# Kernel tuning notes

Hardware: AMD Instinct MI355X
Metric: run time of the kernel (lower is better)

The kernel has to match this reference:

```python
import jax, jax.numpy as jnp
import numpy as np

B, H, L, C, KD, NS = 4, 1024, 8192, 1, 64, 8  # batch, d_model, seq_len, channels, kernel_dim, num_scales
DECAY_MIN, DECAY_MAX = 1.0, 4.0


def _interp_linear(x, scale):
    """F.interpolate(mode='linear', align_corners=False) for integer scale on last axis."""
    if scale == 1:
        return x
    Lin = x.shape[-1]
    Lout = Lin * scale
    pos = (jnp.arange(Lout, dtype=x.dtype) + 0.5) / scale - 0.5
    lo = jnp.floor(pos)
    w = pos - lo  # fractional weight toward hi
    lo_i = jnp.clip(lo.astype(jnp.int32), 0, Lin - 1)
    hi_i = jnp.clip(lo.astype(jnp.int32) + 1, 0, Lin - 1)
    return x[..., lo_i] * (1.0 - w) + x[..., hi_i] * w


def setup_inputs() -> dict:
    key = jax.random.key(0)
    k1, k2, k3, k4 = jax.random.split(key, 4)
    return {
        "u": jax.random.normal(k1, (B, H, L), jnp.float32),
        "kernels": jax.random.normal(k2, (NS, C, H, KD), jnp.float32),
        "D": jax.random.normal(k3, (C, H), jnp.float32),
        "W_out": jax.random.normal(k4, (H, C * H), jnp.float32) / np.sqrt(C * H).astype(np.float32),
        "b_out": jnp.zeros((H,), jnp.float32),
    }


def reference(u, kernels, D, W_out, b_out):
    # --- multi-scale kernel synthesis ('cat' mode, init_scale=0) ---
    mult = jnp.linspace(DECAY_MIN, DECAY_MAX, H).astype(u.dtype).reshape(1, H, 1)
    parts = [
        _interp_linear(kernels[i], 2 ** max(0, i - 1)) * mult ** (NS - 1 - i)
        for i in range(NS)
    ]
    k = jnp.concatenate(parts, axis=-1)  # (C, H, 8192) == (C, H, L) for these dims
    # kernel_norm is computed from the untruncated kernel and detached (buffer)
    knorm = jax.lax.stop_gradient(jnp.linalg.norm(k, axis=-1, keepdims=True))  # (C, H, 1)
    k = k[..., :L] / knorm

    # --- FFT long convolution (causal, via 2L-padded circular conv) ---
    n = 2 * L
    k_f = jnp.fft.rfft(k, n=n)                 # (C, H, L+1) complex
    u_f = jnp.fft.rfft(u, n=n)                 # (B, H, L+1) complex
    y = jnp.fft.irfft(u_f[:, None, :, :] * k_f[None, :, :, :], n=n)[..., :L]  # (B, C, H, L)
    y = y + jnp.einsum('bhl,ch->bchl', u, D)   # skip connection
    y = y.reshape(u.shape[0], C * H, L)        # (B, C*H, L)

    # --- activation + output linear (1x1 conv) ---
    y = jax.nn.gelu(y, approximate=False)      # torch nn.GELU is exact erf form
    y = jnp.einsum('oh,bhl->bol', W_out, y) + b_out[None, :, None]
    return y
```

## Files before the change

### kernel.cpp

```cpp
#include <hip/hip_runtime.h>
#include <hip/hip_bf16.h>

#define LFULL 8192
#define HDIM 1024
#define KPAD 8320

typedef __attribute__((ext_vector_type(8))) short bf16x8;
typedef __attribute__((ext_vector_type(4))) float f32x4;
typedef __attribute__((ext_vector_type(16))) float f32x16;

union U16 {
  uint4 u;
  bf16x8 s;
  ushort e[8];
};

__device__ __forceinline__ ushort f2bf(float x) {
  union { float f; uint u; } a;
  a.f = x;
  uint r = a.u + 0x7fffu + ((a.u >> 16) & 1u);
  return (ushort)(r >> 16);
}
__device__ __forceinline__ float bf2f(ushort x) {
  union { uint u; float f; } a;
  a.u = ((uint)x) << 16;
  return a.f;
}

__device__ __forceinline__ void gload16(const void* src, void* lds) {
  __builtin_amdgcn_global_load_lds(
      (const __attribute__((address_space(1))) unsigned int*)src,
      (__attribute__((address_space(3))) unsigned int*)lds, 16, 0, 0);
}

__device__ __forceinline__ uint ALIGNB(uint hi, uint lo, uint sh) {
#if __has_builtin(__builtin_amdgcn_alignbyte)
  return __builtin_amdgcn_alignbyte(hi, lo, sh);
#else
  return (uint)((((unsigned long long)hi << 32) | (unsigned long long)lo) >> (8u * sh));
#endif
}

__global__ __launch_bounds__(256) void k_synth_kernel(
    const float* __restrict__ kern, ushort* __restrict__ kout) {
  const int h = blockIdx.x;
  const int tid = threadIdx.x;
  __shared__ float Kw[8][64];
  __shared__ __align__(16) float kv[LFULL];
  __shared__ float red[8];
  for (int idx = tid; idx < 8 * 64; idx += 256) {
    int i = idx >> 6, j = idx & 63;
    Kw[i][j] = kern[(i * HDIM + h) * 64 + j];
  }
  __syncthreads();
  const float mult = (float)(1.0 + 3.0 * (double)h / 1023.0);
  float pw[8];
  pw[7] = 1.0f;
#pragma unroll
  for (int i = 6; i >= 0; --i) pw[i] = pw[i + 1] * mult;
  float ss = 0.0f;
  for (int m = tid; m < LFULL; m += 256) {
    const int i = (m < 64) ? 0 : (32 - __clz(m >> 6));
    const int slog = (i == 0) ? 0 : (i - 1);
    const float inv_s = 1.0f / (float)(1 << slog);
    const int off = (i == 0) ? 0 : (64 << (i - 1));
    const int t = m - off;
    const float pos = ((float)t + 0.5f) * inv_s - 0.5f;
    const float lof = floorf(pos);
    const float wgt = pos - lof;
    int lo = (int)lof;
    int hi = lo + 1;
    lo = min(63, max(0, lo));
    hi = min(63, max(0, hi));
    const float val = (Kw[i][lo] * (1.0f - wgt) + Kw[i][hi] * wgt) * pw[i];
    kv[m] = val;
    ss += val * val;
  }
#pragma unroll
  for (int o = 32; o > 0; o >>= 1) ss += __shfl_xor(ss, o, 64);
  if ((tid & 63) == 0) red[tid >> 6] = ss;
  __syncthreads();
  if (tid == 0) red[0] = sqrtf(red[0] + red[1] + red[2] + red[3]);
  __syncthreads();
  const float inv_norm = 1.0f / red[0];
  ushort* krow = kout + (size_t)h * KPAD;
  for (int m = tid; m < LFULL; m += 256) krow[8191 - m] = f2bf(kv[m] * inv_norm);
  if (tid < 128) krow[8192 + tid] = 0;
}

__global__ __launch_bounds__(256, 2) void conv_mfma_kernel(
    const float* __restrict__ u, const ushort* __restrict__ kbrev,
    const float* __restrict__ Dp, ushort* __restrict__ g) {
  __shared__ __align__(16) ushort Us[4 * LFULL];
  __shared__ __align__(16) ushort Ring[4][640];
  const int tid = threadIdx.x;
  const int h = blockIdx.x;
  const int w = tid >> 6;
  const int lane = tid & 63;
  const int c32 = lane & 31;
  const int qh = lane >> 5;
  uint4* Us4 = (uint4*)Us;

  for (int cc = tid; cc < 4096; cc += 256) {
    const int row = cc >> 10, cI = cc & 1023;
    const float* up = u + (((size_t)(row * HDIM + h)) << 13) + (cI << 3);
    const float4 v0 = *(const float4*)up;
    const float4 v1 = *(const float4*)(up + 4);
    U16 pk;
    pk.e[0] = f2bf(v0.x); pk.e[1] = f2bf(v0.y);
    pk.e[2] = f2bf(v0.z); pk.e[3] = f2bf(v0.w);
    pk.e[4] = f2bf(v1.x); pk.e[5] = f2bf(v1.y);
    pk.e[6] = f2bf(v1.z); pk.e[7] = f2bf(v1.w);
    const int phys = (cI & ~7) | ((cI & 7) ^ ((cI >> 3) & 7));
    Us4[(row << 10) + phys] = pk.u;
  }

  const ushort* kr = kbrev + (size_t)h * KPAD;
  ushort* ring = (ushort*)Ring[w];
  {
    const uint k64 = *(const uint*)(kr + 64 * 128 + 2 * lane);
    const uint k63 = *(const uint*)(kr + 63 * 128 + 2 * lane);
    const uint k62 = *(const uint*)(kr + 62 * 128 + 2 * lane);
    *(uint*)(ring + 0 * 128 + 2 * lane) = k64;
    *(uint*)(ring + 512 + 2 * lane) = k64;
    *(uint*)(ring + 3 * 128 + 2 * lane) = k63;
    *(uint*)(ring + 2 * 128 + 2 * lane) = k62;
  }
  uint kreg = *(const uint*)(kr + 61 * 128 + 2 * lane);
  __syncthreads();

  f32x16 acc[4][2];
#pragma unroll
  for (int f = 0; f < 4; ++f)
#pragma unroll
    for (int rg = 0; rg < 2; ++rg)
#pragma unroll
      for (int q = 0; q < 16; ++q) acc[f][rg][q] = 0.0f;

  const uint shby = ((uint)((c32 & 1) ^ 1)) * 2u;
  int Pb = 8191 - c32 + 8 * qh;
  int dcnt = 61;

  for (int d = 0; d < 128; ++d) {
    if ((d & 1) == 0) {
      const int cw = dcnt < 0 ? 0 : dcnt;
      const int slot = (cw & 3) * 128;
      *(uint*)(ring + slot + 2 * lane) = kreg;
      *(uint*)(ring + ((slot == 0) ? 512 : slot) + 2 * lane) = kreg;
      const int cn = (dcnt - 1) < 0 ? 0 : (dcnt - 1);
      kreg = *(const uint*)(kr + cn * 128 + 2 * lane);
      dcnt--;
    }
    bf16x8 W[6];
#pragma unroll
    for (int mm = 0; mm < 6; ++mm) {
      const int P = Pb + 48 - 16 * mm;
      const int pos = (P & ~1) & 511;
      const ushort* rp = ring + pos;
      const uint dw0 = *(const uint*)(rp);
      const uint dw1 = *(const uint*)(rp + 2);
      const uint dw2 = *(const uint*)(rp + 4);
      const uint dw3 = *(const uint*)(rp + 6);
      const uint dw4 = *(const uint*)(rp + 8);
      U16 wv;
      wv.u.x = ALIGNB(dw1, dw0, shby);
      wv.u.y = ALIGNB(dw2, dw1, shby);
      wv.u.z = ALIGNB(dw3, dw2, shby);
      wv.u.w = ALIGNB(dw4, dw3, shby);
      W[mm] = wv.s;
    }
    const int dc = d >> 5, dl = d & 31;
#pragma unroll
    for (int f = 0; f < 4; ++f) {
      if (f >= dc) {
        const int j0 = f * 32 + c32 - d;
        const int jc = j0 < 0 ? 0 : j0;
        const int m8 = jc & 7;
        const uint4* ub = Us4 + (w << 10) + (jc << 3);
        uint4 B[4];
#pragma unroll
        for (int ks = 0; ks < 4; ++ks) B[ks] = ub[(2 * ks + qh) ^ m8];
        if (f == dc && dl != 0) {
          const bool kp = (c32 >= dl);
#pragma unroll
          for (int ks = 0; ks < 4; ++ks) {
            B[ks].x = kp ? B[ks].x : 0u;
            B[ks].y = kp ? B[ks].y : 0u;
            B[ks].z = kp ? B[ks].z : 0u;
            B[ks].w = kp ? B[ks].w : 0u;
          }
        }
#pragma unroll
        for (int rg = 0; rg < 2; ++rg) {
#pragma unroll
          for (int ks = 0; ks < 4; ++ks) {
            U16 bb;
            bb.u = B[ks];
            acc[f][rg] = __builtin_amdgcn_mfma_f32_32x32x16_bf16(
                W[2 * rg - ks + 3], bb.s, acc[f][rg], 0, 0, 0);
          }
        }
      }
    }
    Pb -= 64;
  }

  const float Dh = Dp[h];
  ushort* gp = g + (((size_t)(w * HDIM + h)) << 13);
#pragma unroll
  for (int f = 0; f < 4; ++f) {
#pragma unroll
    for (int rg = 0; rg < 2; ++rg) {
      const int lbase = (f * 32 + c32) * 64 + rg * 32 + 4 * qh;
#pragma unroll
      for (int rq = 0; rq < 4; ++rq) {
        const int l = lbase + 8 * rq;
        const int cI = l >> 3;
        const int phys = (cI & ~7) | ((cI & 7) ^ ((cI >> 3) & 7));
        const uint2 uv =
            *(const uint2*)(Us + (w << 13) + (phys << 3) + 4 * qh);
        float uu[4];
        uu[0] = bf2f((ushort)(uv.x & 0xffff));
        uu[1] = bf2f((ushort)(uv.x >> 16));
        uu[2] = bf2f((ushort)(uv.y & 0xffff));
        uu[3] = bf2f((ushort)(uv.y >> 16));
        ushort o[4];
#pragma unroll
        for (int jj = 0; jj < 4; ++jj) {
          const float y = acc[f][rg][rq * 4 + jj] + Dh * uu[jj];
          const float ge = 0.5f * y * (1.0f + erff(y * 0.70710678118654752f));
          o[jj] = f2bf(ge);
        }
        uint2 op;
        op.x = (uint)o[0] | ((uint)o[1] << 16);
        op.y = (uint)o[2] | ((uint)o[3] << 16);
        *(uint2*)(gp + l) = op;
      }
    }
  }
}

__global__ __launch_bounds__(256) void transpose_kernel(
    const ushort* __restrict__ g, ushort* __restrict__ gt) {
  __shared__ __align__(16) ushort Ts[64 * 64];
  const int l0 = blockIdx.x * 64, hh0 = blockIdx.y * 64, b = blockIdx.z;
  const int tid = threadIdx.x;
#pragma unroll
  for (int p = 0; p < 2; ++p) {
    const int hh = (tid >> 3) + 32 * p;
    const int c8 = tid & 7;
    const uint4 v = *(const uint4*)(g + (((size_t)(b * HDIM + hh0 + hh)) << 13)
                                    + l0 + c8 * 8);
    ((uint4*)Ts)[hh * 8 + (c8 ^ ((hh >> 3) & 7))] = v;
  }
  __syncthreads();
#pragma unroll
  for (int p = 0; p < 2; ++p) {
    const int lr = (tid >> 3) + 32 * p;
    const int o8 = tid & 7;
    U16 pk;
#pragma unroll
    for (int j = 0; j < 8; ++j) {
      const int hq = o8 * 8 + j;
      pk.e[j] = Ts[hq * 64 + (((lr >> 3) ^ o8) << 3) + (lr & 7)];
    }
    ((uint4*)(gt + ((size_t)b * LFULL + l0 + lr) * HDIM + hh0))[o8] = pk.u;
  }
}

__global__ __launch_bounds__(256) void wcvt_kernel(const float* __restrict__ W,
                                                   ushort* __restrict__ Wb) {
  const int i = (blockIdx.x * 256 + threadIdx.x) * 8;
  const float4 v0 = *(const float4*)(W + i);
  const float4 v1 = *(const float4*)(W + i + 4);
  U16 pk;
  pk.e[0] = f2bf(v0.x); pk.e[1] = f2bf(v0.y);
  pk.e[2] = f2bf(v0.z); pk.e[3] = f2bf(v0.w);
  pk.e[4] = f2bf(v1.x); pk.e[5] = f2bf(v1.y);
  pk.e[6] = f2bf(v1.z); pk.e[7] = f2bf(v1.w);
  ((uint4*)Wb)[i >> 3] = pk.u;
}

__global__ __launch_bounds__(256, 2) void outmm_kernel(
    const ushort* __restrict__ Wb, const ushort* __restrict__ gt,
    const float* __restrict__ bo, float* __restrict__ out) {
  __shared__ __align__(16) ushort As[128 * 32];
  __shared__ __align__(16) ushort Bs[128 * 32];
  const int tid = threadIdx.x;
  const int l0 = blockIdx.x * 128, o0 = blockIdx.y * 128, b = blockIdx.z;
  const int w = tid >> 6, lane = tid & 63;
  const int wm = w >> 1, wn = w & 1;
  const int col = lane & 15, q = lane >> 4;
  const int srow = lane >> 2, scol = (lane & 3) * 8;
  f32x4 acc[4][4];
#pragma unroll
  for (int m = 0; m < 4; ++m)
#pragma unroll
    for (int n = 0; n < 4; ++n) acc[m][n] = (f32x4){0.f, 0.f, 0.f, 0.f};
  const ushort* gb = gt + ((size_t)b * LFULL) * HDIM;
  for (int kt = 0; kt < 32; ++kt) {
    const int k0 = kt * 32;
    const int r0 = w * 32;
#pragma unroll
    for (int ii = 0; ii < 2; ++ii) {
      const int ra = r0 + ii * 16 + srow;
      gload16(Wb + (size_t)(o0 + ra) * HDIM + k0 + scol,
              As + (r0 + ii * 16) * 32);
      gload16(gb + (size_t)(l0 + ra) * HDIM + k0 + scol,
              Bs + (r0 + ii * 16) * 32);
    }
    __syncthreads();
    bf16x8 aa[4], bb[4];
#pragma unroll
    for (int m = 0; m < 4; ++m) {
      aa[m] = ((const bf16x8*)As)[(wm * 64 + m * 16 + col) * 4 + q];
      bb[m] = ((const bf16x8*)Bs)[(wn * 64 + m * 16 + col) * 4 + q];
    }
#pragma unroll
    for (int m = 0; m < 4; ++m)
#pragma unroll
      for (int n = 0; n < 4; ++n)
        acc[m][n] = __builtin_amdgcn_mfma_f32_16x16x32_bf16(aa[m], bb[n],
                                                            acc[m][n], 0, 0, 0);
    __syncthreads();
  }
#pragma unroll
  for (int m = 0; m < 4; ++m) {
    const int ob = o0 + wm * 64 + m * 16 + q * 4;
    const float4 bv = *(const float4*)(bo + ob);
    const float bva[4] = {bv.x, bv.y, bv.z, bv.w};
#pragma unroll
    for (int n = 0; n < 4; ++n) {
      const int l = l0 + wn * 64 + n * 16 + col;
      float* op = out + (((size_t)(b * HDIM + ob)) << 13) + l;
#pragma unroll
      for (int v = 0; v < 4; ++v) op[(size_t)v << 13] = acc[m][n][v] + bva[v];
    }
  }
}

extern "C" void kernel_launch(void* const* d_in, const int* in_sizes, int n_in,
                              void* d_out, int out_size, void* d_ws,
                              size_t ws_size, hipStream_t stream) {
  const float* u = (const float*)d_in[0];
  const float* kern = (const float*)d_in[1];
  const float* D = (const float*)d_in[2];
  const float* W = (const float*)d_in[3];
  const float* bo = (const float*)d_in[4];
  float* out = (float*)d_out;

  char* ws = (char*)d_ws;
  ushort* g = (ushort*)ws;
  ushort* gt = (ushort*)(ws + ((size_t)64 << 20));
  ushort* kbrev = (ushort*)(ws + ((size_t)128 << 20));
  ushort* Wb = (ushort*)(ws + ((size_t)128 << 20));

  k_synth_kernel<<<HDIM, 256, 0, stream>>>(kern, kbrev);
  conv_mfma_kernel<<<HDIM, 256, 0, stream>>>(u, kbrev, D, g);
  wcvt_kernel<<<512, 256, 0, stream>>>(W, Wb);
  transpose_kernel<<<dim3(128, 16, 4), 256, 0, stream>>>(g, gt);
  outmm_kernel<<<dim3(64, 8, 4), 256, 0, stream>>>(Wb, gt, bo, out);
}
```

Before: 480.0 us.

## Retile MFMA causal convolution to 128-wide blocks with double-buffered Toeplitz fragments

Changes the Toeplitz block decomposition from 64-sample blocks (4x2 accumulator tiles, 128 diagonal steps) to 128-sample blocks (2x4 tiles, 64 diagonal steps). Kernel fragments built at one step are reused at the next through alternating register buffers WA/WB, so only 8 new fragments are built per step. The LDS swizzle and the kernel ring buffer are widened to match. This cuts loop overhead and LDS reads for the kernel operand per MFMA. In exchange it raises register pressure (30 uint4 fragment buffers) and does more wasted MFMA work on the masked diagonal blocks.

Measured after the change: 482.9 us. About the same (+0.6%).

```diff
diff --git a/kernel.cpp b/kernel.cpp
--- a/kernel.cpp
+++ b/kernel.cpp
@@ -3,7 +3,7 @@
 
 #define LFULL 8192
 #define HDIM 1024
-#define KPAD 8320
+#define KPAD 8448
 
 typedef __attribute__((ext_vector_type(8))) short bf16x8;
 typedef __attribute__((ext_vector_type(4))) float f32x4;
@@ -40,6 +40,8 @@
   return (uint)((((unsigned long long)hi << 32) | (unsigned long long)lo) >> (8u * sh));
 #endif
 }
+
+#define USWZ16(cI) ((cI) ^ (((cI) >> 4) & 15))
 
 __global__ __launch_bounds__(256) void k_synth_kernel(
     const float* __restrict__ kern, ushort* __restrict__ kout) {
@@ -85,14 +87,14 @@
   const float inv_norm = 1.0f / red[0];
   ushort* krow = kout + (size_t)h * KPAD;
   for (int m = tid; m < LFULL; m += 256) krow[8191 - m] = f2bf(kv[m] * inv_norm);
-  if (tid < 128) krow[8192 + tid] = 0;
+  if (tid < 256) krow[8192 + tid] = 0;
 }
 
 __global__ __launch_bounds__(256, 2) void conv_mfma_kernel(
     const float* __restrict__ u, const ushort* __restrict__ kbrev,
     const float* __restrict__ Dp, ushort* __restrict__ g) {
   __shared__ __align__(16) ushort Us[4 * LFULL];
-  __shared__ __align__(16) ushort Ring[4][640];
+  __shared__ __align__(16) ushort Ring[4][1152];
   const int tid = threadIdx.x;
   const int h = blockIdx.x;
   const int w = tid >> 6;
@@ -111,114 +113,124 @@
     pk.e[2] = f2bf(v0.z); pk.e[3] = f2bf(v0.w);
     pk.e[4] = f2bf(v1.x); pk.e[5] = f2bf(v1.y);
     pk.e[6] = f2bf(v1.z); pk.e[7] = f2bf(v1.w);
-    const int phys = (cI & ~7) | ((cI & 7) ^ ((cI >> 3) & 7));
-    Us4[(row << 10) + phys] = pk.u;
+    Us4[(row << 10) + USWZ16(cI)] = pk.u;
   }
 
   const ushort* kr = kbrev + (size_t)h * KPAD;
-  ushort* ring = (ushort*)Ring[w];
+  char* ringb = (char*)Ring[w];
   {
-    const uint k64 = *(const uint*)(kr + 64 * 128 + 2 * lane);
-    const uint k63 = *(const uint*)(kr + 63 * 128 + 2 * lane);
-    const uint k62 = *(const uint*)(kr + 62 * 128 + 2 * lane);
-    *(uint*)(ring + 0 * 128 + 2 * lane) = k64;
-    *(uint*)(ring + 512 + 2 * lane) = k64;
-    *(uint*)(ring + 3 * 128 + 2 * lane) = k63;
-    *(uint*)(ring + 2 * 128 + 2 * lane) = k62;
-  }
-  uint kreg = *(const uint*)(kr + 61 * 128 + 2 * lane);
-  __syncthreads();
-
-  f32x16 acc[4][2];
-#pragma unroll
-  for (int f = 0; f < 4; ++f)
-#pragma unroll
-    for (int rg = 0; rg < 2; ++rg)
+    const uint kc65 = *(const uint*)(kr + 65 * 128 + 2 * lane);
+    const uint kc64 = *(const uint*)(kr + 64 * 128 + 2 * lane);
+    const uint kc63 = *(const uint*)(kr + 63 * 128 + 2 * lane);
+    *(uint*)(ringb + 1 * 256 + 4 * lane) = kc65;
+    *(uint*)(ringb + 0 * 256 + 4 * lane) = kc64;
+    *(uint*)(ringb + 2048 + 4 * lane) = kc64;
+    *(uint*)(ringb + 7 * 256 + 4 * lane) = kc63;
+  }
+  uint kreg = *(const uint*)(kr + 62 * 128 + 2 * lane);
+  __syncthreads();
+
+  f32x16 acc[2][4];
+#pragma unroll
+  for (int f = 0; f < 2; ++f)
+#pragma unroll
+    for (int rg = 0; rg < 4; ++rg)
 #pragma unroll
       for (int q = 0; q < 16; ++q) acc[f][rg][q] = 0.0f;
 
-  const uint shby = ((uint)((c32 & 1) ^ 1)) * 2u;
-  int Pb = 8191 - c32 + 8 * qh;
-  int dcnt = 61;
-
-  for (int d = 0; d < 128; ++d) {
-    if ((d & 1) == 0) {
-      const int cw = dcnt < 0 ? 0 : dcnt;
-      const int slot = (cw & 3) * 128;
-      *(uint*)(ring + slot + 2 * lane) = kreg;
-      *(uint*)(ring + ((slot == 0) ? 512 : slot) + 2 * lane) = kreg;
-      const int cn = (dcnt - 1) < 0 ? 0 : (dcnt - 1);
-      kreg = *(const uint*)(kr + cn * 128 + 2 * lane);
-      dcnt--;
-    }
-    bf16x8 W[6];
-#pragma unroll
-    for (int mm = 0; mm < 6; ++mm) {
-      const int P = Pb + 48 - 16 * mm;
-      const int pos = (P & ~1) & 511;
-      const ushort* rp = ring + pos;
-      const uint dw0 = *(const uint*)(rp);
-      const uint dw1 = *(const uint*)(rp + 2);
-      const uint dw2 = *(const uint*)(rp + 4);
-      const uint dw3 = *(const uint*)(rp + 6);
-      const uint dw4 = *(const uint*)(rp + 8);
-      U16 wv;
-      wv.u.x = ALIGNB(dw1, dw0, shby);
-      wv.u.y = ALIGNB(dw2, dw1, shby);
-      wv.u.z = ALIGNB(dw3, dw2, shby);
-      wv.u.w = ALIGNB(dw4, dw3, shby);
-      W[mm] = wv.s;
-    }
-    const int dc = d >> 5, dl = d & 31;
-#pragma unroll
-    for (int f = 0; f < 4; ++f) {
-      if (f >= dc) {
-        const int j0 = f * 32 + c32 - d;
-        const int jc = j0 < 0 ? 0 : j0;
-        const int m8 = jc & 7;
-        const uint4* ub = Us4 + (w << 10) + (jc << 3);
-        uint4 B[4];
-#pragma unroll
-        for (int ks = 0; ks < 4; ++ks) B[ks] = ub[(2 * ks + qh) ^ m8];
-        if (f == dc && dl != 0) {
-          const bool kp = (c32 >= dl);
-#pragma unroll
-          for (int ks = 0; ks < 4; ++ks) {
-            B[ks].x = kp ? B[ks].x : 0u;
-            B[ks].y = kp ? B[ks].y : 0u;
-            B[ks].z = kp ? B[ks].z : 0u;
-            B[ks].w = kp ? B[ks].w : 0u;
-          }
-        }
-#pragma unroll
-        for (int rg = 0; rg < 2; ++rg) {
-#pragma unroll
-          for (int ks = 0; ks < 4; ++ks) {
-            U16 bb;
-            bb.u = B[ks];
-            acc[f][rg] = __builtin_amdgcn_mfma_f32_32x32x16_bf16(
-                W[2 * rg - ks + 3], bb.s, acc[f][rg], 0, 0, 0);
-          }
-        }
-      }
-    }
-    Pb -= 64;
+  const int PBASE = 8191 - c32 + 8 * qh;
+  const bool s8 = ((PBASE >> 1) & 1) != 0;
+  const uint sh = 2u * (uint)(PBASE & 1);
+
+  uint4 WA[15], WB[15];
+
+#define BUILD_W(DD, MM, DST) {                                          \
+    const int P = PBASE + 128 - 128 * (DD) - 16 * (MM);                 \
+    const int LL = (2 * (P & 1023)) & ~7;                               \
+    const uint2 r0 = *(const uint2*)(ringb + LL);                       \
+    const uint2 r1 = *(const uint2*)(ringb + LL + 8);                   \
+    const uint2 r2 = *(const uint2*)(ringb + LL + 16);                  \
+    const uint v0 = s8 ? r0.y : r0.x;                                   \
+    const uint v1 = s8 ? r1.x : r0.y;                                   \
+    const uint v2 = s8 ? r1.y : r1.x;                                   \
+    const uint v3 = s8 ? r2.x : r1.y;                                   \
+    const uint v4 = s8 ? r2.y : r2.x;                                   \
+    (DST).x = ALIGNB(v1, v0, sh);                                       \
+    (DST).y = ALIGNB(v2, v1, sh);                                       \
+    (DST).z = ALIGNB(v3, v2, sh);                                       \
+    (DST).w = ALIGNB(v4, v3, sh); }
+
+#define WGET(Wc, Wf, MM) ((MM) >= 7 ? (Wf)[(MM)] : (Wc)[(MM) + 8])
+
+#define FPART(DD, F, DIAG, Wc, Wf) {                                    \
+    const int j0 = (F) * 32 + c32 - (DD);                               \
+    const int jc = j0 < 0 ? 0 : j0;                                     \
+    const uint zmask = ((DIAG) && (j0 < 0)) ? 0u : 0xffffffffu;         \
+    _Pragma("unroll")                                                   \
+    for (int ks = 0; ks < 8; ++ks) {                                    \
+      const int cI = 16 * jc + 2 * ks + qh;                             \
+      U16 bb;                                                           \
+      bb.u = Us4[(w << 10) + USWZ16(cI)];                               \
+      if (DIAG) {                                                       \
+        bb.u.x &= zmask; bb.u.y &= zmask;                               \
+        bb.u.z &= zmask; bb.u.w &= zmask;                               \
+      }                                                                 \
+      U16 a0, a1, a2, a3;                                               \
+      a0.u = WGET(Wc, Wf, 8 - ks);                                      \
+      a1.u = WGET(Wc, Wf, 10 - ks);                                     \
+      a2.u = WGET(Wc, Wf, 12 - ks);                                     \
+      a3.u = WGET(Wc, Wf, 14 - ks);                                     \
+      acc[F][0] = __builtin_amdgcn_mfma_f32_32x32x16_bf16(a0.s, bb.s, acc[F][0], 0, 0, 0); \
+      acc[F][1] = __builtin_amdgcn_mfma_f32_32x32x16_bf16(a1.s, bb.s, acc[F][1], 0, 0, 0); \
+      acc[F][2] = __builtin_amdgcn_mfma_f32_32x32x16_bf16(a2.s, bb.s, acc[F][2], 0, 0, 0); \
+      acc[F][3] = __builtin_amdgcn_mfma_f32_32x32x16_bf16(a3.s, bb.s, acc[F][3], 0, 0, 0); \
+    } }
+
+#define CONV_STEP(DD, Wc, Wf, HASF0) {                                  \
+    _Pragma("unroll")                                                   \
+    for (int mm = 7; mm <= 14; ++mm) BUILD_W(DD, mm, (Wf)[mm]);         \
+    {                                                                   \
+      const int cw0 = 62 - (DD);                                        \
+      const int cw = cw0 < 0 ? 0 : cw0;                                 \
+      const int sl = (cw & 7) * 256;                                    \
+      *(uint*)(ringb + sl + 4 * lane) = kreg;                           \
+      *(uint*)(ringb + ((sl == 0) ? 2048 : sl) + 4 * lane) = kreg;      \
+      const int cn0 = 61 - (DD);                                        \
+      const int cn = cn0 < 0 ? 0 : cn0;                                 \
+      kreg = *(const uint*)(kr + cn * 128 + 2 * lane);                  \
+    }                                                                   \
+    if (HASF0) {                                                        \
+      FPART(DD, 0, true, Wc, Wf);                                       \
+      FPART(DD, 1, false, Wc, Wf);                                      \
+    } else {                                                            \
+      FPART(DD, 1, true, Wc, Wf);                                       \
+    } }
+
+#pragma unroll
+  for (int mm = 1; mm <= 6; ++mm) BUILD_W(0, mm, WB[mm + 8]);
+
+  for (int dd = 0; dd < 32; dd += 2) {
+    CONV_STEP(dd, WB, WA, true);
+    CONV_STEP(dd + 1, WA, WB, true);
+  }
+  for (int dd = 32; dd < 64; dd += 2) {
+    CONV_STEP(dd, WB, WA, false);
+    CONV_STEP(dd + 1, WA, WB, false);
   }
 
   const float Dh = Dp[h];
   ushort* gp = g + (((size_t)(w * HDIM + h)) << 13);
 #pragma unroll
-  for (int f = 0; f < 4; ++f) {
-#pragma unroll
-    for (int rg = 0; rg < 2; ++rg) {
-      const int lbase = (f * 32 + c32) * 64 + rg * 32 + 4 * qh;
+  for (int f = 0; f < 2; ++f) {
+#pragma unroll
+    for (int rg = 0; rg < 4; ++rg) {
+      const int lbase = (f * 32 + c32) * 128 + rg * 32 + 4 * qh;
 #pragma unroll
       for (int rq = 0; rq < 4; ++rq) {
         const int l = lbase + 8 * rq;
         const int cI = l >> 3;
-        const int phys = (cI & ~7) | ((cI & 7) ^ ((cI >> 3) & 7));
-        const uint2 uv =
-            *(const uint2*)(Us + (w << 13) + (phys << 3) + 4 * qh);
+        const int phys = USWZ16(cI);
+        const uint2 uv = *(const uint2*)(Us + (w << 13) + (phys << 3) + 4 * qh);
         float uu[4];
         uu[0] = bf2f((ushort)(uv.x & 0xffff));
         uu[1] = bf2f((ushort)(uv.x >> 16));
```
